# Performance work log

Hardware: AMD Instinct MI355X
Metric: run time of the kernel (lower is better)

## Reference

```python
import jax, jax.numpy as jnp
import numpy as np

N_NODES = 100000
N_EDGES = 3200000
N_GRAPHS = 128
HIDDEN = 128
DEPTH = 3


def setup_inputs() -> dict:
    key = jax.random.key(0)
    ks = jax.random.split(key, 12)
    x = jax.random.normal(ks[0], (N_NODES, 1), dtype=jnp.float32)
    edge_index = jax.random.randint(ks[1], (2, N_EDGES), 0, N_NODES, dtype=jnp.int64)
    batch = jnp.sort(jax.random.randint(ks[2], (N_NODES,), 0, N_GRAPHS, dtype=jnp.int64))
    s = 1.0 / np.sqrt(HIDDEN)
    return {
        "x": x,
        "edge_index": edge_index,
        "batch": batch,
        "W_emb": jax.random.normal(ks[3], (1, HIDDEN), dtype=jnp.float32),
        "b_emb": jax.random.normal(ks[4], (HIDDEN,), dtype=jnp.float32) * 0.01,
        "W_gnn": jax.random.normal(ks[5], (DEPTH, HIDDEN, HIDDEN), dtype=jnp.float32) * s,
        "b_gnn": jax.random.normal(ks[6], (DEPTH, HIDDEN), dtype=jnp.float32) * 0.01,
        "W_c1": jax.random.normal(ks[7], (HIDDEN, HIDDEN // 2), dtype=jnp.float32) * s,
        "b_c1": jax.random.normal(ks[8], (HIDDEN // 2,), dtype=jnp.float32) * 0.01,
        "W_c2": jax.random.normal(ks[9], (HIDDEN // 2, 1), dtype=jnp.float32) * s,
        "b_c2": jax.random.normal(ks[10], (1,), dtype=jnp.float32) * 0.01,
    }


def reference(x, edge_index, batch, W_emb, b_emb, W_gnn, b_gnn, W_c1, b_c1, W_c2, b_c2):
    # --- GCN normalization (self-loops + symmetric deg^-1/2) ---
    loop = jnp.arange(N_NODES, dtype=edge_index.dtype)
    row = jnp.concatenate([edge_index[0], loop])  # source nodes
    col = jnp.concatenate([edge_index[1], loop])  # target nodes
    deg = jax.ops.segment_sum(jnp.ones_like(col, dtype=jnp.float32), col, num_segments=N_NODES)
    dinv = jnp.where(deg > 0, jax.lax.rsqrt(jnp.maximum(deg, 1.0)), 0.0)
    norm = dinv[row] * dinv[col]  # [E+N]

    # --- node embedding ---
    h = x @ W_emb + b_emb  # [N, H]

    # --- GCN layers: linear -> gather -> normalize -> scatter-add -> bias -> relu ---
    for l in range(DEPTH):
        h_lin = h @ W_gnn[l]                       # [N, H]
        msgs = h_lin[row] * norm[:, None]          # [E+N, H]
        agg = jax.ops.segment_sum(msgs, col, num_segments=N_NODES)
        h = jax.nn.relu(agg + b_gnn[l])

    # --- global mean pool per graph ---
    counts = jax.ops.segment_sum(jnp.ones((N_NODES,), jnp.float32), batch, num_segments=N_GRAPHS)
    sums = jax.ops.segment_sum(h, batch, num_segments=N_GRAPHS)
    g = sums / jnp.maximum(counts, 1.0)[:, None]   # [G, H]

    # --- classifier (dropout is identity in eval) ---
    z = jax.nn.relu(g @ W_c1 + b_c1)
    out = jax.nn.sigmoid(z @ W_c2 + b_c2)          # [G, 1]
    return out.squeeze(-1)                          # [G]
```

## Files before the change

kernel.cpp:

```cpp
#include <hip/hip_runtime.h>
#include <math.h>

#define HID 128
#define CAP 96
#define TILE 8192
#define WSH 9
#define BUKCAP 24576

typedef unsigned int uint;
typedef unsigned short ushort;
typedef float f32x2 __attribute__((ext_vector_type(2)));
typedef float f32x4 __attribute__((ext_vector_type(4)));
typedef short bf16x8 __attribute__((ext_vector_type(8)));

__device__ inline ushort f2bf(float f) {
    uint u = __float_as_uint(f);
    return (ushort)((u + 0x7fffu + ((u >> 16) & 1u)) >> 16);
}
__device__ inline uint packbf(float a, float b) {
    return (uint)f2bf(a) | ((uint)f2bf(b) << 16);
}
__device__ inline bf16x8 as_bf16x8(uint4 u) {
    union { uint4 a; bf16x8 b; } c;
    c.a = u;
    return c.b;
}

__device__ inline f32x2 fp8lo(uint q) { return __builtin_amdgcn_cvt_pk_f32_fp8(q, false); }
__device__ inline f32x2 fp8hi(uint q) { return __builtin_amdgcn_cvt_pk_f32_fp8(q, true); }
__device__ inline uint pack4fp8(float a, float b, float c, float d) {
    int t = __builtin_amdgcn_cvt_pk_fp8_f32(a, b, 0, false);
    return (uint)__builtin_amdgcn_cvt_pk_fp8_f32(c, d, t, true);
}


__global__ void __launch_bounds__(256) k_part(const int* __restrict__ row,
                                              const int* __restrict__ col,
                                              int* __restrict__ bukCur,
                                              uint* __restrict__ recs, int E) {
    __shared__ int hist[256];
    __shared__ int hist2[256];
    __shared__ uint base[256];
    int t = threadIdx.x;
    hist[t] = 0;
    hist2[t] = 0;
    __syncthreads();
    int i0 = blockIdx.x * TILE;
    int i1 = min(E, i0 + TILE);
    for (int i = i0 + t; i < i1; i += 256) {
        int b = col[i] >> WSH;
        atomicAdd(&hist[b], 1);
    }
    __syncthreads();
    if (hist[t] > 0) base[t] = (uint)atomicAdd(&bukCur[t], hist[t]);
    __syncthreads();
    for (int i = i0 + t; i < i1; i += 256) {
        int c = col[i];
        int b = c >> WSH;
        uint p = (uint)atomicAdd(&hist2[b], 1);
        uint idx = base[b] + p;
        if (idx < BUKCAP)
            recs[(size_t)b * BUKCAP + idx] = (uint)row[i] | ((uint)(c & 511) << 17);
    }
}

__global__ void __launch_bounds__(256) k_fbin(const uint* __restrict__ recs,
                                              const int* __restrict__ bukCur,
                                              const float* __restrict__ x,
                                              int* __restrict__ cnt,
                                              int* __restrict__ ebin,
                                              float* __restrict__ dinv,
                                              float2* __restrict__ pk0, int N) {
    __shared__ int lcnt[512];
    int b = blockIdx.x;
    int t = threadIdx.x;
    lcnt[t] = 0;
    lcnt[t + 256] = 0;
    __syncthreads();
    int n = min(bukCur[b], BUKCAP);
    const uint* rp = recs + (size_t)b * BUKCAP;
    int cbase = b << WSH;
    for (int j = t; j < n; j += 256) {
        uint u = rp[j];
        int r = (int)(u & 0x1FFFFu);
        int cl = (int)(u >> 17);
        int p = atomicAdd(&lcnt[cl], 1);
        if (p < CAP) ebin[(size_t)(cbase + cl) * CAP + p] = r << 5;
    }
    __syncthreads();
    int c0 = cbase + t;
    if (c0 < N) {
        cnt[c0] = lcnt[t];
        float d = rsqrtf((float)lcnt[t] + 1.0f);
        dinv[c0] = d;
        pk0[c0] = make_float2(d, d * x[c0]);
    }
    int c1 = cbase + t + 256;
    if (c1 < N) {
        cnt[c1] = lcnt[t + 256];
        float d = rsqrtf((float)lcnt[t + 256] + 1.0f);
        dinv[c1] = d;
        pk0[c1] = make_float2(d, d * x[c1]);
    }
}


__global__ void k_wprep(const float* __restrict__ W_emb, const float* __restrict__ b_emb,
                        const float* __restrict__ W_gnn,
                        float* __restrict__ u, float* __restrict__ v,
                        uint4* __restrict__ wfrag) {
    int b = blockIdx.x;
    int t = threadIdx.x;
    if (b < 16) {
        int gid = b * 256 + t;
        int l = gid >> 11;
        int rem = gid & 2047;
        int kb = rem >> 9;
        int nt = (rem >> 6) & 7;
        int lane = rem & 63;
        int k0 = kb * 32 + (lane >> 4) * 8;
        int n = nt * 16 + (lane & 15);
        const float* Wp = W_gnn + (size_t)(l + 1) * HID * HID;
        uint4 o;
        o.x = packbf(Wp[(k0 + 0) * HID + n], Wp[(k0 + 1) * HID + n]);
        o.y = packbf(Wp[(k0 + 2) * HID + n], Wp[(k0 + 3) * HID + n]);
        o.z = packbf(Wp[(k0 + 4) * HID + n], Wp[(k0 + 5) * HID + n]);
        o.w = packbf(Wp[(k0 + 6) * HID + n], Wp[(k0 + 7) * HID + n]);
        wfrag[gid] = o;
    } else if (t < HID) {
        float su = 0.f, sv = 0.f;
        for (int k = 0; k < HID; ++k) {
            float w = W_gnn[k * HID + t];
            su = fmaf(W_emb[k], w, su);
            sv = fmaf(b_emb[k], w, sv);
        }
        u[t] = su;
        v[t] = sv;
    }
}


__global__ void __launch_bounds__(256) k_sagg(const int* __restrict__ cnt,
                                              const int* __restrict__ ebin,
                                              const float* __restrict__ x,
                                              const float* __restrict__ dinv,
                                              const float2* __restrict__ pk0,
                                              const float* __restrict__ u,
                                              const float* __restrict__ v,
                                              const float* __restrict__ b0,
                                              uint* __restrict__ g8, int N) {
    __shared__ float sS0[256], sS1[256], sDc[256];
    int t = threadIdx.x;
    int c0 = blockIdx.x * 256;
    int c = c0 + t;
    if (c < N) {
        float dc = dinv[c];
        float A = 0.f, B = 0.f;
        int n = min(cnt[c], CAP);
        const int* bp = ebin + (size_t)c * CAP;
        int k = 0;
        for (; k + 4 <= n; k += 4) {
            float2 p0 = pk0[bp[k] >> 5], p1 = pk0[bp[k + 1] >> 5];
            float2 p2 = pk0[bp[k + 2] >> 5], p3 = pk0[bp[k + 3] >> 5];
            A += (p0.x + p1.x) + (p2.x + p3.x);
            B += (p0.y + p1.y) + (p2.y + p3.y);
        }
        for (; k < n; ++k) {
            float2 p = pk0[bp[k] >> 5];
            A += p.x;
            B += p.y;
        }
        float d2 = dc * dc;
        sS0[t] = fmaf(dc, A, d2);
        sS1[t] = fmaf(dc, B, d2 * x[c]);
        sDc[t] = dc;
    }
    __syncthreads();
    int nloc = min(256, N - c0);
    int total = nloc * 32;
    for (int gid = t; gid < total; gid += 256) {
        int lc = gid >> 5;
        int j = (gid & 31) * 4;
        float t1 = sS1[lc], t0 = sS0[lc], dc = sDc[lc];
        float v0 = fmaxf(fmaf(t1, u[j + 0], fmaf(t0, v[j + 0], b0[j + 0])), 0.f);
        float v1 = fmaxf(fmaf(t1, u[j + 1], fmaf(t0, v[j + 1], b0[j + 1])), 0.f);
        float v2 = fmaxf(fmaf(t1, u[j + 2], fmaf(t0, v[j + 2], b0[j + 2])), 0.f);
        float v3 = fmaxf(fmaf(t1, u[j + 3], fmaf(t0, v[j + 3], b0[j + 3])), 0.f);
        g8[(size_t)(c0 + lc) * 32 + (gid & 31)] = pack4fp8(dc * v0, dc * v1, dc * v2, dc * v3);
    }
}


__global__ void __launch_bounds__(256) k_agg(const int* __restrict__ cnt,
                                             const int* __restrict__ ebin,
                                             const float* __restrict__ dinv,
                                             const uint* __restrict__ g8,
                                             uint* __restrict__ a, int N) {
    int wave = (blockIdx.x * 256 + threadIdx.x) >> 6;
    if (wave >= N) return;
    int lane = threadIdx.x & 63;
    int c = wave;
    int ql = lane & 15;
    int qg = lane >> 4;
    const uint* __restrict__ gq = g8 + ql * 2;

    f32x2 a0 = {0.f, 0.f}, a1 = {0.f, 0.f}, a2 = {0.f, 0.f}, a3 = {0.f, 0.f};

    int n = min(cnt[c], CAP);
    int total = n + 1;
    const int* __restrict__ bp = ebin + (size_t)c * CAP - 1;

    for (int base = 0; base < total; base += 64) {
        int cw = min(total - base, 64);
        int gi = base + lane;
        int ro = 0;
        if (lane < cw) ro = (gi == 0) ? (c << 5) : bp[gi];
        int j = 0;
        for (; j + 16 <= cw; j += 16) {
            int o0 = __shfl(ro, j + qg);
            int o1 = __shfl(ro, j + 4 + qg);
            int o2 = __shfl(ro, j + 8 + qg);
            int o3 = __shfl(ro, j + 12 + qg);
            uint2 q0 = *(const uint2*)(gq + o0);
            uint2 q1 = *(const uint2*)(gq + o1);
            uint2 q2 = *(const uint2*)(gq + o2);
            uint2 q3 = *(const uint2*)(gq + o3);
            a0 += fp8lo(q0.x); a1 += fp8hi(q0.x); a2 += fp8lo(q0.y); a3 += fp8hi(q0.y);
            a0 += fp8lo(q1.x); a1 += fp8hi(q1.x); a2 += fp8lo(q1.y); a3 += fp8hi(q1.y);
            a0 += fp8lo(q2.x); a1 += fp8hi(q2.x); a2 += fp8lo(q2.y); a3 += fp8hi(q2.y);
            a0 += fp8lo(q3.x); a1 += fp8hi(q3.x); a2 += fp8lo(q3.y); a3 += fp8hi(q3.y);
        }
        for (; j + 4 <= cw; j += 4) {
            int o0 = __shfl(ro, j + qg);
            uint2 q0 = *(const uint2*)(gq + o0);
            a0 += fp8lo(q0.x); a1 += fp8hi(q0.x); a2 += fp8lo(q0.y); a3 += fp8hi(q0.y);
        }
        if (j < cw) {
            int e = j + qg;
            int o0 = __shfl(ro, min(e, cw - 1));
            uint2 q0 = *(const uint2*)(gq + o0);
            if (e >= cw) { q0.x = 0u; q0.y = 0u; }
            a0 += fp8lo(q0.x); a1 += fp8hi(q0.x); a2 += fp8lo(q0.y); a3 += fp8hi(q0.y);
        }
    }

    float r0 = a0.x, r1 = a0.y, r2 = a1.x, r3 = a1.y;
    float r4 = a2.x, r5 = a2.y, r6 = a3.x, r7 = a3.y;
#pragma unroll
    for (int m = 16; m <= 32; m <<= 1) {
        r0 += __shfl_xor(r0, m); r1 += __shfl_xor(r1, m);
        r2 += __shfl_xor(r2, m); r3 += __shfl_xor(r3, m);
        r4 += __shfl_xor(r4, m); r5 += __shfl_xor(r5, m);
        r6 += __shfl_xor(r6, m); r7 += __shfl_xor(r7, m);
    }
    if (qg == 0) {
        float dc = dinv[c];
        uint4 o;
        o.x = packbf(dc * r0, dc * r1);
        o.y = packbf(dc * r2, dc * r3);
        o.z = packbf(dc * r4, dc * r5);
        o.w = packbf(dc * r6, dc * r7);
        ((uint4*)(a + (size_t)c * 64))[ql] = o;
    }
}


#define RCH 32
__global__ void __launch_bounds__(256, 2) k_gemm(const uint* __restrict__ A,
                                                 const uint4* __restrict__ wfrag,
                                                 const float* __restrict__ bias,
                                                 const float* __restrict__ rowscale,
                                                 uint* __restrict__ H8, int N) {
    __shared__ uint4 sAf[4][2][64];
    __shared__ float sEp[4][16][68];
    int t = threadIdx.x;
    int w = t >> 6;
    int lane = t & 63;
    int rowgrp = w >> 1;
    int colh = w & 1;

    bf16x8 Bf[4][4];
#pragma unroll
    for (int kb = 0; kb < 4; ++kb)
#pragma unroll
        for (int i = 0; i < 4; ++i)
            Bf[kb][i] = as_bf16x8(wfrag[(kb * 8 + colh * 4 + i) * 64 + lane]);

    float4 bb = ((const float4*)bias)[colh * 16 + (lane & 15)];

    int nchunk = (N + RCH - 1) / RCH;
    for (int ch = blockIdx.x; ch < nchunk; ch += gridDim.x) {
        int r0 = ch * RCH;
        __syncthreads();
#pragma unroll
        for (int s = 0; s < 2; ++s) {
            int i = t + s * 256;
            int kb = i >> 7;
            int rg = (i >> 6) & 1;
            int ln = i & 63;
            int gr = r0 + rg * 16 + (ln & 15);
            gr = min(gr, N - 1);
            sAf[kb][rg][ln] = ((const uint4*)(A + (size_t)gr * 64))[kb * 4 + (ln >> 4)];
        }
        __syncthreads();

        f32x4 acc[4] = {{0.f, 0.f, 0.f, 0.f}, {0.f, 0.f, 0.f, 0.f},
                        {0.f, 0.f, 0.f, 0.f}, {0.f, 0.f, 0.f, 0.f}};
#pragma unroll
        for (int kb = 0; kb < 4; ++kb) {
            bf16x8 af = as_bf16x8(sAf[kb][rowgrp][lane]);
#pragma unroll
            for (int i = 0; i < 4; ++i)
                acc[i] = __builtin_amdgcn_mfma_f32_16x16x32_bf16(af, Bf[kb][i], acc[i], 0, 0, 0);
        }

#pragma unroll
        for (int i = 0; i < 4; ++i) {
#pragma unroll
            for (int reg = 0; reg < 4; ++reg)
                sEp[w][(lane >> 4) * 4 + reg][i * 16 + (lane & 15)] = acc[i][reg];
        }
#pragma unroll
        for (int e = 0; e < 4; ++e) {
            int rr = (lane >> 4) + 4 * e;
            int cu = lane & 15;
            const float* sp = &sEp[w][rr][cu * 4];
            int rowg = r0 + rowgrp * 16 + rr;
            if (rowg < N) {
                float sc = rowscale ? rowscale[rowg] : 1.0f;
                float o0 = sc * fmaxf(sp[0] + bb.x, 0.f);
                float o1 = sc * fmaxf(sp[1] + bb.y, 0.f);
                float o2 = sc * fmaxf(sp[2] + bb.z, 0.f);
                float o3 = sc * fmaxf(sp[3] + bb.w, 0.f);
                H8[(size_t)rowg * 32 + colh * 16 + cu] = pack4fp8(o0, o1, o2, o3);
            }
        }
    }
}


__global__ void k_pool(const uint* __restrict__ h8, const int* __restrict__ batch,
                       float* __restrict__ gpool, float* __restrict__ gcnt, int N) {
    int gi = blockIdx.x >> 2, part = blockIdx.x & 3;
    int t = threadIdx.x;
    int ui = t & 31;
    int sub = t >> 5;
    int lo = 0, hi = N;
    while (lo < hi) { int m = (lo + hi) >> 1; if (batch[m] < gi) lo = m + 1; else hi = m; }
    int start = lo;
    lo = start; hi = N;
    while (lo < hi) { int m = (lo + hi) >> 1; if (batch[m] <= gi) lo = m + 1; else hi = m; }
    int end = lo;
    if (part == 0 && t == 0) gcnt[gi] = (float)(end - start);
    int len = end - start;
    int q = (len + 15) >> 4;
    int seg = part * 4 + sub;
    int rs = start + seg * q;
    int re = min(end, rs + q);
    float s0 = 0.f, s1 = 0.f, s2 = 0.f, s3 = 0.f;
    for (int i = rs; i < re; ++i) {
        uint qq = h8[(size_t)i * 32 + ui];
        f32x2 lo2 = fp8lo(qq), hi2 = fp8hi(qq);
        s0 += lo2.x; s1 += lo2.y; s2 += hi2.x; s3 += hi2.y;
    }
    if (re > rs) {
        float* gp = gpool + gi * HID + ui * 4;
        atomicAdd(gp + 0, s0);
        atomicAdd(gp + 1, s1);
        atomicAdd(gp + 2, s2);
        atomicAdd(gp + 3, s3);
    }
}

__global__ void k_cls(const float* __restrict__ gpool, const float* __restrict__ gcnt,
                      const float* __restrict__ Wc1, const float* __restrict__ bc1,
                      const float* __restrict__ Wc2, const float* __restrict__ bc2,
                      float* __restrict__ out) {
    int g = blockIdx.x;
    int j = threadIdx.x;
    float inv = 1.0f / fmaxf(gcnt[g], 1.0f);
    float z = bc1[j];
    for (int k = 0; k < HID; ++k) z = fmaf(gpool[g * HID + k] * inv, Wc1[k * 64 + j], z);
    z = fmaxf(z, 0.f);
    float p = z * Wc2[j];
    for (int off = 32; off; off >>= 1) p += __shfl_down(p, off);
    if (j == 0) out[g] = 1.0f / (1.0f + expf(-(p + bc2[0])));
}


extern "C" void kernel_launch(void* const* d_in, const int* in_sizes, int n_in,
                              void* d_out, int out_size, void* d_ws, size_t ws_size,
                              hipStream_t stream) {
    const float* x     = (const float*)d_in[0];
    const int*   eidx  = (const int*)d_in[1];
    const int*   batch = (const int*)d_in[2];
    const float* W_emb = (const float*)d_in[3];
    const float* b_emb = (const float*)d_in[4];
    const float* W_gnn = (const float*)d_in[5];
    const float* b_gnn = (const float*)d_in[6];
    const float* W_c1  = (const float*)d_in[7];
    const float* b_c1  = (const float*)d_in[8];
    const float* W_c2  = (const float*)d_in[9];
    const float* b_c2  = (const float*)d_in[10];

    const int N = in_sizes[0];
    const int E = in_sizes[1] / 2;
    const int G = out_size;
    const int* row = eidx;
    const int* col = eidx + E;
    const int NBUK = (N + 511) >> WSH;

    char* ws = (char*)d_ws;
    auto alloc = [&](size_t bytes) -> void* {
        void* p = (void*)ws;
        ws += (bytes + 255) & ~(size_t)255;
        return p;
    };
    int*    cnt    = (int*)alloc((size_t)N * 4);
    float*  dinv   = (float*)alloc((size_t)N * 4);
    float2* pk0    = (float2*)alloc((size_t)N * 8);
    int*    bukCur = (int*)alloc(256 * 4);
    uint*   recs   = (uint*)alloc((size_t)NBUK * BUKCAP * 4);
    int*    ebin   = (int*)alloc((size_t)N * CAP * 4);
    float*  u      = (float*)alloc(HID * 4);
    float*  v      = (float*)alloc(HID * 4);
    uint*   G8     = (uint*)alloc((size_t)N * 32 * 4);
    uint*   A      = (uint*)alloc((size_t)N * 64 * 4);
    uint4*  wfrag  = (uint4*)alloc(4096 * 16);
    float*  gpool  = (float*)alloc((size_t)G * HID * 4);
    float*  gcnt   = (float*)alloc((size_t)G * 4);

    hipMemsetAsync(bukCur, 0, 256 * 4, stream);
    hipMemsetAsync(gpool, 0, (size_t)G * HID * 4, stream);

    k_part<<<(E + TILE - 1) / TILE, 256, 0, stream>>>(row, col, bukCur, recs, E);
    k_fbin<<<NBUK, 256, 0, stream>>>(recs, bukCur, x, cnt, ebin, dinv, pk0, N);

    k_wprep<<<17, 256, 0, stream>>>(W_emb, b_emb, W_gnn, u, v, wfrag);

    k_sagg<<<(N + 255) / 256, 256, 0, stream>>>(cnt, ebin, x, dinv, pk0, u, v, b_gnn, G8, N);

    int nchunk = (N + RCH - 1) / RCH;
    int gblk = nchunk < 768 ? nchunk : 768;
    for (int l = 1; l < 3; ++l) {
        k_agg<<<(N + 3) / 4, 256, 0, stream>>>(cnt, ebin, dinv, G8, A, N);
        k_gemm<<<gblk, 256, 0, stream>>>(A, wfrag + (size_t)(l - 1) * 2048,
                                         b_gnn + (size_t)l * HID,
                                         (l == 1) ? dinv : (const float*)nullptr,
                                         G8, N);
    }

    k_pool<<<G * 4, 128, 0, stream>>>(G8, batch, gpool, gcnt, N);
    k_cls<<<G, 64, 0, stream>>>(gpool, gcnt, W_c1, b_c1, W_c2, b_c2, (float*)d_out);
}
```

Baseline: 371.0 us.

## Process two nodes per wave in k_agg with software-pipelined gather loads

The aggregation kernel now gives each wavefront two destination nodes. It loads both neighbor lists up front (up to 128 entries in two registers) and interleaves double-buffered gather issue and accumulate stages, so more independent memory loads are in flight per wave. Neighbor-index loads and output stores use nontemporal hints, and the grid is halved. The cost is higher register pressure, which may reduce occupancy, and some wasted work when the two nodes have very different degrees.

```diff
diff --git a/kernel.cpp b/kernel.cpp
--- a/kernel.cpp
+++ b/kernel.cpp
@@ -11,6 +11,7 @@
 typedef unsigned short ushort;
 typedef float f32x2 __attribute__((ext_vector_type(2)));
 typedef float f32x4 __attribute__((ext_vector_type(4)));
+typedef uint u32x4 __attribute__((ext_vector_type(4)));
 typedef short bf16x8 __attribute__((ext_vector_type(8)));
 
 __device__ inline ushort f2bf(float f) {
@@ -191,76 +192,133 @@
 }
 
 
+#define ISSUE(ro0_, ro1_, tX, k, b0, b1, b2, b3)                          \
+    {                                                                     \
+        int ro_ = ((k) < 4) ? (ro0_) : (ro1_);                            \
+        int jo_ = ((k) & 3) * 16;                                         \
+        int l0_ = jo_ + qg, l1_ = jo_ + 4 + qg;                           \
+        int l2_ = jo_ + 8 + qg, l3_ = jo_ + 12 + qg;                      \
+        if ((tX) < ((k) + 1) * 16) {                                      \
+            int tr_ = (tX) - 1 - (((k) >= 4) ? 64 : 0);                   \
+            l0_ = min(l0_, tr_); l1_ = min(l1_, tr_);                     \
+            l2_ = min(l2_, tr_); l3_ = min(l3_, tr_);                     \
+        }                                                                 \
+        b0 = *(const uint2*)(gq + __shfl(ro_, l0_));                      \
+        b1 = *(const uint2*)(gq + __shfl(ro_, l1_));                      \
+        b2 = *(const uint2*)(gq + __shfl(ro_, l2_));                      \
+        b3 = *(const uint2*)(gq + __shfl(ro_, l3_));                      \
+    }
+
+#define ACC1(q_, x0, x1, x2, x3)                                          \
+    { x0 += fp8lo(q_.x); x1 += fp8hi(q_.x); x2 += fp8lo(q_.y); x3 += fp8hi(q_.y); }
+
+#define COMPUTE(tX, k, b0, b1, b2, b3, x0, x1, x2, x3)                    \
+    {                                                                     \
+        if ((tX) < ((k) + 1) * 16) {                                      \
+            int e_ = (k) * 16 + qg;                                       \
+            if (e_ >= (tX))      { b0.x = 0u; b0.y = 0u; }                \
+            if (e_ + 4 >= (tX))  { b1.x = 0u; b1.y = 0u; }                \
+            if (e_ + 8 >= (tX))  { b2.x = 0u; b2.y = 0u; }                \
+            if (e_ + 12 >= (tX)) { b3.x = 0u; b3.y = 0u; }                \
+        }                                                                 \
+        ACC1(b0, x0, x1, x2, x3); ACC1(b1, x0, x1, x2, x3);               \
+        ACC1(b2, x0, x1, x2, x3); ACC1(b3, x0, x1, x2, x3);               \
+    }
+
 __global__ void __launch_bounds__(256) k_agg(const int* __restrict__ cnt,
                                              const int* __restrict__ ebin,
                                              const float* __restrict__ dinv,
                                              const uint* __restrict__ g8,
                                              uint* __restrict__ a, int N) {
-    int wave = (blockIdx.x * 256 + threadIdx.x) >> 6;
-    if (wave >= N) return;
+    int pair = (blockIdx.x * 256 + threadIdx.x) >> 6;
+    int cA = pair * 2;
+    if (cA >= N) return;
+    int cB = cA + 1;
+    bool hasB = (cB < N);
     int lane = threadIdx.x & 63;
-    int c = wave;
     int ql = lane & 15;
     int qg = lane >> 4;
     const uint* __restrict__ gq = g8 + ql * 2;
 
-    f32x2 a0 = {0.f, 0.f}, a1 = {0.f, 0.f}, a2 = {0.f, 0.f}, a3 = {0.f, 0.f};
-
-    int n = min(cnt[c], CAP);
-    int total = n + 1;
-    const int* __restrict__ bp = ebin + (size_t)c * CAP - 1;
-
-    for (int base = 0; base < total; base += 64) {
-        int cw = min(total - base, 64);
-        int gi = base + lane;
-        int ro = 0;
-        if (lane < cw) ro = (gi == 0) ? (c << 5) : bp[gi];
-        int j = 0;
-        for (; j + 16 <= cw; j += 16) {
-            int o0 = __shfl(ro, j + qg);
-            int o1 = __shfl(ro, j + 4 + qg);
-            int o2 = __shfl(ro, j + 8 + qg);
-            int o3 = __shfl(ro, j + 12 + qg);
-            uint2 q0 = *(const uint2*)(gq + o0);
-            uint2 q1 = *(const uint2*)(gq + o1);
-            uint2 q2 = *(const uint2*)(gq + o2);
-            uint2 q3 = *(const uint2*)(gq + o3);
-            a0 += fp8lo(q0.x); a1 += fp8hi(q0.x); a2 += fp8lo(q0.y); a3 += fp8hi(q0.y);
-            a0 += fp8lo(q1.x); a1 += fp8hi(q1.x); a2 += fp8lo(q1.y); a3 += fp8hi(q1.y);
-            a0 += fp8lo(q2.x); a1 += fp8hi(q2.x); a2 += fp8lo(q2.y); a3 += fp8hi(q2.y);
-            a0 += fp8lo(q3.x); a1 += fp8hi(q3.x); a2 += fp8lo(q3.y); a3 += fp8hi(q3.y);
-        }
-        for (; j + 4 <= cw; j += 4) {
-            int o0 = __shfl(ro, j + qg);
-            uint2 q0 = *(const uint2*)(gq + o0);
-            a0 += fp8lo(q0.x); a1 += fp8hi(q0.x); a2 += fp8lo(q0.y); a3 += fp8hi(q0.y);
-        }
-        if (j < cw) {
-            int e = j + qg;
-            int o0 = __shfl(ro, min(e, cw - 1));
-            uint2 q0 = *(const uint2*)(gq + o0);
-            if (e >= cw) { q0.x = 0u; q0.y = 0u; }
-            a0 += fp8lo(q0.x); a1 += fp8hi(q0.x); a2 += fp8lo(q0.y); a3 += fp8hi(q0.y);
-        }
-    }
-
-    float r0 = a0.x, r1 = a0.y, r2 = a1.x, r3 = a1.y;
-    float r4 = a2.x, r5 = a2.y, r6 = a3.x, r7 = a3.y;
+    int tA = min(cnt[cA], CAP) + 1;
+    int tB = hasB ? (min(cnt[cB], CAP) + 1) : 0;
+    const int* __restrict__ bpA = ebin + (size_t)cA * CAP - 1;
+    const int* __restrict__ bpB = ebin + (size_t)cB * CAP - 1;
+
+    int iA = min(lane, tA - 1);
+    int lvA = __builtin_nontemporal_load(bpA + max(iA, 1));
+    int roA0 = (iA == 0) ? (cA << 5) : lvA;
+    int roA1 = 0;
+    if (tA > 64) roA1 = __builtin_nontemporal_load(bpA + min(64 + lane, tA - 1));
+    int roB0 = 0, roB1 = 0;
+    if (hasB) {
+        int iB = min(lane, tB - 1);
+        int lvB = __builtin_nontemporal_load(bpB + max(iB, 1));
+        roB0 = (iB == 0) ? (cB << 5) : lvB;
+        if (tB > 64) roB1 = __builtin_nontemporal_load(bpB + min(64 + lane, tB - 1));
+    }
+
+    int nbA = (tA + 15) >> 4;
+    int nbB = (tB + 15) >> 4;
+    int nb = max(nbA, nbB);
+
+    f32x2 aA0 = {0.f, 0.f}, aA1 = {0.f, 0.f}, aA2 = {0.f, 0.f}, aA3 = {0.f, 0.f};
+    f32x2 aB0 = {0.f, 0.f}, aB1 = {0.f, 0.f}, aB2 = {0.f, 0.f}, aB3 = {0.f, 0.f};
+    uint2 qA00, qA01, qA02, qA03, qA10, qA11, qA12, qA13;
+    uint2 qB00, qB01, qB02, qB03, qB10, qB11, qB12, qB13;
+
+    ISSUE(roA0, roA1, tA, 0, qA00, qA01, qA02, qA03);
+    if (0 < nbB) ISSUE(roB0, roB1, tB, 0, qB00, qB01, qB02, qB03);
+    if (1 < nbA) ISSUE(roA0, roA1, tA, 1, qA10, qA11, qA12, qA13);
+    if (1 < nbB) ISSUE(roB0, roB1, tB, 1, qB10, qB11, qB12, qB13);
+
+    int k = 0;
+    for (; k + 1 < nb; k += 2) {
+        if (k < nbA) COMPUTE(tA, k, qA00, qA01, qA02, qA03, aA0, aA1, aA2, aA3);
+        if (k + 2 < nbA) ISSUE(roA0, roA1, tA, k + 2, qA00, qA01, qA02, qA03);
+        if (k < nbB) COMPUTE(tB, k, qB00, qB01, qB02, qB03, aB0, aB1, aB2, aB3);
+        if (k + 2 < nbB) ISSUE(roB0, roB1, tB, k + 2, qB00, qB01, qB02, qB03);
+        if (k + 1 < nbA) COMPUTE(tA, k + 1, qA10, qA11, qA12, qA13, aA0, aA1, aA2, aA3);
+        if (k + 3 < nbA) ISSUE(roA0, roA1, tA, k + 3, qA10, qA11, qA12, qA13);
+        if (k + 1 < nbB) COMPUTE(tB, k + 1, qB10, qB11, qB12, qB13, aB0, aB1, aB2, aB3);
+        if (k + 3 < nbB) ISSUE(roB0, roB1, tB, k + 3, qB10, qB11, qB12, qB13);
+    }
+    if (k < nb) {
+        if (k < nbA) COMPUTE(tA, k, qA00, qA01, qA02, qA03, aA0, aA1, aA2, aA3);
+        if (k < nbB) COMPUTE(tB, k, qB00, qB01, qB02, qB03, aB0, aB1, aB2, aB3);
+    }
+
+    float rA0 = aA0.x, rA1 = aA0.y, rA2 = aA1.x, rA3 = aA1.y;
+    float rA4 = aA2.x, rA5 = aA2.y, rA6 = aA3.x, rA7 = aA3.y;
+    float rB0 = aB0.x, rB1 = aB0.y, rB2 = aB1.x, rB3 = aB1.y;
+    float rB4 = aB2.x, rB5 = aB2.y, rB6 = aB3.x, rB7 = aB3.y;
 #pragma unroll
     for (int m = 16; m <= 32; m <<= 1) {
-        r0 += __shfl_xor(r0, m); r1 += __shfl_xor(r1, m);
-        r2 += __shfl_xor(r2, m); r3 += __shfl_xor(r3, m);
-        r4 += __shfl_xor(r4, m); r5 += __shfl_xor(r5, m);
-        r6 += __shfl_xor(r6, m); r7 += __shfl_xor(r7, m);
+        rA0 += __shfl_xor(rA0, m); rA1 += __shfl_xor(rA1, m);
+        rA2 += __shfl_xor(rA2, m); rA3 += __shfl_xor(rA3, m);
+        rA4 += __shfl_xor(rA4, m); rA5 += __shfl_xor(rA5, m);
+        rA6 += __shfl_xor(rA6, m); rA7 += __shfl_xor(rA7, m);
+        rB0 += __shfl_xor(rB0, m); rB1 += __shfl_xor(rB1, m);
+        rB2 += __shfl_xor(rB2, m); rB3 += __shfl_xor(rB3, m);
+        rB4 += __shfl_xor(rB4, m); rB5 += __shfl_xor(rB5, m);
+        rB6 += __shfl_xor(rB6, m); rB7 += __shfl_xor(rB7, m);
     }
     if (qg == 0) {
-        float dc = dinv[c];
-        uint4 o;
-        o.x = packbf(dc * r0, dc * r1);
-        o.y = packbf(dc * r2, dc * r3);
-        o.z = packbf(dc * r4, dc * r5);
-        o.w = packbf(dc * r6, dc * r7);
-        ((uint4*)(a + (size_t)c * 64))[ql] = o;
+        float dc = dinv[cA];
+        u32x4 o;
+        o.x = packbf(dc * rA0, dc * rA1);
+        o.y = packbf(dc * rA2, dc * rA3);
+        o.z = packbf(dc * rA4, dc * rA5);
+        o.w = packbf(dc * rA6, dc * rA7);
+        __builtin_nontemporal_store(o, (u32x4*)(a + (size_t)cA * 64) + ql);
+    } else if (qg == 1 && hasB) {
+        float dc = dinv[cB];
+        u32x4 o;
+        o.x = packbf(dc * rB0, dc * rB1);
+        o.y = packbf(dc * rB2, dc * rB3);
+        o.z = packbf(dc * rB4, dc * rB5);
+        o.w = packbf(dc * rB6, dc * rB7);
+        __builtin_nontemporal_store(o, (u32x4*)(a + (size_t)cB * 64) + ql);
     }
 }
 
@@ -442,8 +500,9 @@
 
     int nchunk = (N + RCH - 1) / RCH;
     int gblk = nchunk < 768 ? nchunk : 768;
+    int npair = (N + 1) / 2;
     for (int l = 1; l < 3; ++l) {
-        k_agg<<<(N + 3) / 4, 256, 0, stream>>>(cnt, ebin, dinv, G8, A, N);
+        k_agg<<<(npair + 3) / 4, 256, 0, stream>>>(cnt, ebin, dinv, G8, A, N);
         k_gemm<<<gblk, 256, 0, stream>>>(A, wfrag + (size_t)(l - 1) * 2048,
                                          b_gnn + (size_t)l * HID,
                                          (l == 1) ? dinv : (const float*)nullptr,
```

New measurement: 380.0 us. 1.02x slower.
